# Kernel tuning notes

Measured on AMD Instinct MI355X. Metric: run time of the kernel, lower is better.

Reference implementation:

```python
import jax, jax.numpy as jnp
import numpy as np

D_MODEL = 768
NUM_HEADS = 12
D_K = D_MODEL // NUM_HEADS
B, S = 2, 4096


def setup_inputs() -> dict:
    key = jax.random.key(0)
    ks = jax.random.split(key, 11)
    lim = 1.0 / np.sqrt(D_MODEL)  # torch Linear default init range
    def lin(k1, k2):
        W = jax.random.uniform(k1, (D_MODEL, D_MODEL), jnp.float32, -lim, lim)
        b = jax.random.uniform(k2, (D_MODEL,), jnp.float32, -lim, lim)
        return W, b
    Wq, bq = lin(ks[0], ks[1])
    Wk, bk = lin(ks[2], ks[3])
    Wv, bv = lin(ks[4], ks[5])
    Wo, bo = lin(ks[6], ks[7])
    Q = jax.random.normal(ks[8], (B, S, D_MODEL), jnp.float32)
    K = jax.random.normal(ks[9], (B, S, D_MODEL), jnp.float32)
    V = jax.random.normal(ks[10], (B, S, D_MODEL), jnp.float32)
    return {"Q": Q, "K": K, "V": V,
            "Wq": Wq, "bq": bq, "Wk": Wk, "bk": bk,
            "Wv": Wv, "bv": bv, "Wo": Wo, "bo": bo}


def reference(Q, K, V, Wq, bq, Wk, bk, Wv, bv, Wo, bo):
    def split_heads(x):
        b, s, _ = x.shape
        return x.reshape(b, s, NUM_HEADS, D_K).transpose(0, 2, 1, 3)  # [B,H,S,d_k]

    q = split_heads(Q @ Wq.T + bq)
    k = split_heads(K @ Wk.T + bk)
    v = split_heads(V @ Wv.T + bv)

    scale = 1.0 / np.sqrt(D_K).astype(np.float32)
    scores = jnp.einsum('bhqd,bhkd->bhqk', q, k) * scale  # [B,H,S,S]
    probs = jax.nn.softmax(scores, axis=-1)
    attn = jnp.einsum('bhqk,bhkd->bhqd', probs, v)  # [B,H,S,d_k]

    out = attn.transpose(0, 2, 1, 3).reshape(Q.shape[0], Q.shape[1], D_MODEL)
    return out @ Wo.T + bo
```

## Files before the change

kernel.cpp:

```cpp
#include <hip/hip_runtime.h>
#include <hip/hip_bf16.h>
#include <stdint.h>

#define DM 768
#define DK 64
#define NH 12
#define SQ 4096
#define BB 2

typedef __attribute__((ext_vector_type(8))) short bf16x8;
typedef __attribute__((ext_vector_type(4))) float f32x4;
typedef __attribute__((ext_vector_type(16))) float f32x16;
typedef __attribute__((ext_vector_type(4))) unsigned short u16x4;
typedef __attribute__((ext_vector_type(4))) unsigned int u32x4;
typedef unsigned short u16;
typedef unsigned int   u32;

__device__ __forceinline__ u16 f2bf(float f) {
    u32 u = __builtin_bit_cast(u32, f);
    u32 r = (u + 0x7fffu + ((u >> 16) & 1u)) >> 16;
    return (u16)r;
}
__device__ __forceinline__ u32 pack_trunc(float lo, float hi) {
    return __builtin_amdgcn_perm(__builtin_bit_cast(u32, hi),
                                 __builtin_bit_cast(u32, lo), 0x07060302u);
}
__device__ __forceinline__ void gl_lds16(const u16* g, u16* l) {
    __builtin_amdgcn_global_load_lds(
        (const __attribute__((address_space(1))) void*)g,
        (__attribute__((address_space(3))) void*)l, 16, 0, 0);
}

__global__ __launch_bounds__(256) void cvt_w(
    const float* __restrict__ W0, const float* __restrict__ W1,
    const float* __restrict__ W2, const float* __restrict__ W3,
    u16* __restrict__ d0, u16* __restrict__ d1,
    u16* __restrict__ d2, u16* __restrict__ d3)
{
    const float* s = blockIdx.y == 0 ? W0 : blockIdx.y == 1 ? W1
                   : blockIdx.y == 2 ? W2 : W3;
    u16* d        = blockIdx.y == 0 ? d0 : blockIdx.y == 1 ? d1
                   : blockIdx.y == 2 ? d2 : d3;
    size_t i = ((size_t)blockIdx.x * 256 + threadIdx.x) * 8;
    float4 a = *(const float4*)&s[i];
    float4 b = *(const float4*)&s[i + 4];
    u16x4 lo, hi;
    lo.x = f2bf(a.x); lo.y = f2bf(a.y); lo.z = f2bf(a.z); lo.w = f2bf(a.w);
    hi.x = f2bf(b.x); hi.y = f2bf(b.y); hi.z = f2bf(b.z); hi.w = f2bf(b.w);
    *(u16x4*)&d[i]     = lo;
    *(u16x4*)&d[i + 4] = hi;
}

#define BM 128
#define BN 128

__global__ __launch_bounds__(256) void gemm_qkv(
    const float* __restrict__ A0, const float* __restrict__ A1,
    const float* __restrict__ A2,
    const u16* __restrict__ W0, const u16* __restrict__ W1,
    const u16* __restrict__ W2,
    const float* __restrict__ b0, const float* __restrict__ b1,
    const float* __restrict__ b2,
    u16* __restrict__ qo, u16* __restrict__ ko, u16* __restrict__ vto,
    float qscale)
{
    __shared__ __align__(16) u16 Asm[2][BM * 32];
    __shared__ __align__(16) u16 Bsm[2][BM * 32];

    const int tid  = threadIdx.x;
    const int lane = tid & 63;
    const int w    = tid >> 6;
    const int wr   = w >> 1, wc = w & 1;
    const int l16  = lane & 15, lg = lane >> 4;

    const int ntiles = DM / BN;
    const int mt = blockIdx.x / ntiles;
    const int nt = blockIdx.x % ntiles;
    const int m0 = mt * BM, n0 = nt * BN;

    const int op = blockIdx.y;
    const float* A    = op == 0 ? A0 : op == 1 ? A1 : A2;
    const u16*  W     = op == 0 ? W0 : op == 1 ? W1 : W2;
    const float* bias = op == 0 ? b0 : op == 1 ? b1 : b2;
    const float oscale = op == 0 ? qscale : 1.0f;

    f32x4 acc[4][4];
    #pragma unroll
    for (int mi = 0; mi < 4; ++mi)
        #pragma unroll
        for (int ni = 0; ni < 4; ++ni)
            #pragma unroll
            for (int r = 0; r < 4; ++r) acc[mi][ni][r] = 0.f;

    #define GSTAGE(K0, B)                                                      \
        do {                                                                   \
            _Pragma("unroll")                                                  \
            for (int i_ = 0; i_ < 2; ++i_) {                                   \
                int c_   = (i_ * 4 + w) * 64 + lane;                           \
                int row_ = c_ >> 2;                                            \
                int col_ = ((c_ & 3) ^ (row_ & 3)) * 8;                        \
                gl_lds16(&W[(size_t)(n0 + row_) * DM + (K0) + col_],           \
                         &Bsm[B][(i_ * 4 + w) * 512]);                         \
            }                                                                  \
            _Pragma("unroll")                                                  \
            for (int i_ = 0; i_ < 2; ++i_) {                                   \
                int s_   = tid + i_ * 256;                                     \
                int row_ = s_ >> 2;                                            \
                int col_ = ((s_ & 3) ^ (row_ & 3)) * 8;                        \
                float4 x_ = *(const float4*)&A[(size_t)(m0 + row_) * DM + (K0) + col_];     \
                float4 y_ = *(const float4*)&A[(size_t)(m0 + row_) * DM + (K0) + col_ + 4]; \
                u16x4 lo_, hi_;                                                \
                lo_.x = f2bf(x_.x); lo_.y = f2bf(x_.y);                        \
                lo_.z = f2bf(x_.z); lo_.w = f2bf(x_.w);                        \
                hi_.x = f2bf(y_.x); hi_.y = f2bf(y_.y);                        \
                hi_.z = f2bf(y_.z); hi_.w = f2bf(y_.w);                        \
                *(u16x4*)&Asm[B][s_ * 8]     = lo_;                            \
                *(u16x4*)&Asm[B][s_ * 8 + 4] = hi_;                            \
            }                                                                  \
        } while (0)

    GSTAGE(0, 0);

    for (int kk = 0; kk < DM / 32; ++kk) {
        __syncthreads();
        if (kk + 1 < DM / 32) GSTAGE((kk + 1) * 32, (kk + 1) & 1);

        const u16* Ab = Asm[kk & 1];
        const u16* Bb = Bsm[kk & 1];
        bf16x8 af[4], bfr[4];
        #pragma unroll
        for (int mi = 0; mi < 4; ++mi) {
            int r = wr * 64 + mi * 16 + l16;
            af[mi] = *(const bf16x8*)((const char*)Ab + (size_t)r * 64
                                      + (((lg ^ r) & 3) << 4));
        }
        #pragma unroll
        for (int ni = 0; ni < 4; ++ni) {
            int r = wc * 64 + ni * 16 + l16;
            bfr[ni] = *(const bf16x8*)((const char*)Bb + (size_t)r * 64
                                       + (((lg ^ r) & 3) << 4));
        }

        #pragma unroll
        for (int mi = 0; mi < 4; ++mi)
            #pragma unroll
            for (int ni = 0; ni < 4; ++ni)
                acc[mi][ni] = __builtin_amdgcn_mfma_f32_16x16x32_bf16(
                    af[mi], bfr[ni], acc[mi][ni], 0, 0, 0);
    }
    #undef GSTAGE

    #pragma unroll
    for (int mi = 0; mi < 4; ++mi)
        #pragma unroll
        for (int ni = 0; ni < 4; ++ni) {
            int n = n0 + wc * 64 + ni * 16 + l16;
            float bv = bias[n];
            if (op == 2) {
                int hh = n >> 6, dd = n & 63;
                int mb = m0 + wr * 64 + mi * 16 + lg * 4;
                int bI = mb >> 12;
                int kv = mb & (SQ - 1);
                u16x4 pk;
                #pragma unroll
                for (int r = 0; r < 4; ++r)
                    pk[r] = f2bf(acc[mi][ni][r] + bv);
                *(u16x4*)&vto[(((size_t)bI * NH + hh) * DK + dd) * SQ + kv] = pk;
            } else {
                u16* out = op ? ko : qo;
                #pragma unroll
                for (int r = 0; r < 4; ++r) {
                    int m = m0 + wr * 64 + mi * 16 + lg * 4 + r;
                    out[(size_t)m * DM + n] = f2bf((acc[mi][ni][r] + bv) * oscale);
                }
            }
        }
}

__global__ __launch_bounds__(256) void gemm_out(
    const u16* __restrict__ A, const u16* __restrict__ W,
    const float* __restrict__ bias, float* __restrict__ C)
{
    __shared__ __align__(16) u16 Asm[2][BM * 32];
    __shared__ __align__(16) u16 Bsm[2][BM * 32];

    const int tid  = threadIdx.x;
    const int lane = tid & 63;
    const int w    = tid >> 6;
    const int wr   = w >> 1, wc = w & 1;
    const int l16  = lane & 15, lg = lane >> 4;

    const int ntiles = DM / BN;
    const int mt = blockIdx.x / ntiles;
    const int nt = blockIdx.x % ntiles;
    const int m0 = mt * BM, n0 = nt * BN;

    f32x4 acc[4][4];
    #pragma unroll
    for (int mi = 0; mi < 4; ++mi)
        #pragma unroll
        for (int ni = 0; ni < 4; ++ni)
            #pragma unroll
            for (int r = 0; r < 4; ++r) acc[mi][ni][r] = 0.f;

    #define OSTAGE(K0, B)                                                      \
        do {                                                                   \
            _Pragma("unroll")                                                  \
            for (int i_ = 0; i_ < 2; ++i_) {                                   \
                int c_   = (i_ * 4 + w) * 64 + lane;                           \
                int row_ = c_ >> 2;                                            \
                int col_ = ((c_ & 3) ^ (row_ & 3)) * 8;                        \
                gl_lds16(&W[(size_t)(n0 + row_) * DM + (K0) + col_],           \
                         &Bsm[B][(i_ * 4 + w) * 512]);                         \
                gl_lds16(&A[(size_t)(m0 + row_) * DM + (K0) + col_],           \
                         &Asm[B][(i_ * 4 + w) * 512]);                         \
            }                                                                  \
        } while (0)

    OSTAGE(0, 0);

    for (int kk = 0; kk < DM / 32; ++kk) {
        __syncthreads();
        if (kk + 1 < DM / 32) OSTAGE((kk + 1) * 32, (kk + 1) & 1);

        const u16* Ab = Asm[kk & 1];
        const u16* Bb = Bsm[kk & 1];
        bf16x8 af[4], bfr[4];
        #pragma unroll
        for (int mi = 0; mi < 4; ++mi) {
            int r = wr * 64 + mi * 16 + l16;
            af[mi] = *(const bf16x8*)((const char*)Ab + (size_t)r * 64
                                      + (((lg ^ r) & 3) << 4));
        }
        #pragma unroll
        for (int ni = 0; ni < 4; ++ni) {
            int r = wc * 64 + ni * 16 + l16;
            bfr[ni] = *(const bf16x8*)((const char*)Bb + (size_t)r * 64
                                       + (((lg ^ r) & 3) << 4));
        }

        #pragma unroll
        for (int mi = 0; mi < 4; ++mi)
            #pragma unroll
            for (int ni = 0; ni < 4; ++ni)
                acc[mi][ni] = __builtin_amdgcn_mfma_f32_16x16x32_bf16(
                    af[mi], bfr[ni], acc[mi][ni], 0, 0, 0);
    }
    #undef OSTAGE

    #pragma unroll
    for (int mi = 0; mi < 4; ++mi)
        #pragma unroll
        for (int ni = 0; ni < 4; ++ni) {
            int n = n0 + wc * 64 + ni * 16 + l16;
            float bv = bias[n];
            #pragma unroll
            for (int r = 0; r < 4; ++r) {
                int m = m0 + wr * 64 + mi * 16 + lg * 4 + r;
                C[(size_t)m * DM + n] = acc[mi][ni][r] + bv;
            }
        }
}

__global__ __launch_bounds__(512) void flash_attn_db(
    const u16* __restrict__ Qm, const u16* __restrict__ Km,
    const u16* __restrict__ VT, u16* __restrict__ Om)
{
    __shared__ __align__(16) char ldsbuf[65536];

    const int tid  = threadIdx.x;
    const int lane = tid & 63;
    const int w    = tid >> 6;
    const int qg   = w & 3;
    const int half = w >> 2;
    const int kvL  = lane & 31;
    const int hi   = lane >> 5;

    const int qt = blockIdx.x;
    const int bh = blockIdx.y;
    const int b  = bh / NH, h = bh % NH;
    const size_t baseQ  = (size_t)b * SQ * DM + (size_t)h * DK;
    const size_t baseVT = (size_t)bh * DK * SQ;

    const int q = qt * 128 + qg * 32 + kvL;

    bf16x8 qf[4];
    #pragma unroll
    for (int j = 0; j < 4; ++j)
        qf[j] = *(const bf16x8*)&Qm[baseQ + (size_t)q * DM + j * 16 + hi * 8];

    int off[4];
    #pragma unroll
    for (int j = 0; j < 4; ++j)
        off[j] = kvL * 128 + (((2 * j + hi) ^ (kvL & 7)) << 4);

    int srow[2], schk[2];
    #pragma unroll
    for (int i = 0; i < 2; ++i) {
        int r = (qg * 2 + i) * 8 + (lane >> 3);
        srow[i] = r;
        schk[i] = (((lane & 7) ^ (r & 7)) << 3);
    }

    f32x16 accO[2];
    #pragma unroll
    for (int e = 0; e < 16; ++e) { accO[0][e] = 0.f; accO[1][e] = 0.f; }
    float lrun = 0.f;

    #define STAGE(T, B)                                                        \
        do {                                                                   \
            int kv0_ = (T) * 128 + half * 64;                                  \
            u16* KL_ = (u16*)(ldsbuf + (B) * 32768 + half * 16384);            \
            u16* VL_ = (u16*)(ldsbuf + (B) * 32768 + half * 16384 + 8192);     \
            _Pragma("unroll")                                                  \
            for (int i_ = 0; i_ < 2; ++i_) {                                   \
                gl_lds16(&Km[baseQ + (size_t)(kv0_ + srow[i_]) * DM + schk[i_]], \
                         KL_ + (qg * 2 + i_) * 512);                           \
                gl_lds16(&VT[baseVT + (size_t)srow[i_] * SQ + kv0_ + schk[i_]], \
                         VL_ + (qg * 2 + i_) * 512);                           \
            }                                                                  \
        } while (0)

    STAGE(0, 0);

    for (int t = 0; t < SQ / 128; ++t) {
        __syncthreads();
        if (t + 1 < SQ / 128) STAGE(t + 1, (t + 1) & 1);

        const char* KB = ldsbuf + (t & 1) * 32768 + half * 16384;
        const char* VB = KB + 8192;

        f32x16 s0, s1;
        #pragma unroll
        for (int e = 0; e < 16; ++e) { s0[e] = 0.f; s1[e] = 0.f; }
        __builtin_amdgcn_s_setprio(1);
        #pragma unroll
        for (int j = 0; j < 4; ++j) {
            bf16x8 kf0 = *(const bf16x8*)(KB + off[j]);
            bf16x8 kf1 = *(const bf16x8*)(KB + 4096 + off[j]);
            s0 = __builtin_amdgcn_mfma_f32_32x32x16_bf16(kf0, qf[j], s0, 0, 0, 0);
            s1 = __builtin_amdgcn_mfma_f32_32x32x16_bf16(kf1, qf[j], s1, 0, 0, 0);
        }
        __builtin_amdgcn_s_setprio(0);

        bf16x8 vf0[4], vf1[4];
        #pragma unroll
        for (int m = 0; m < 4; ++m) {
            vf0[m] = *(const bf16x8*)(VB + off[m]);
            vf1[m] = *(const bf16x8*)(VB + 4096 + off[m]);
        }

        u32 pb[16];
        float rs0 = 0.f, rs1 = 0.f;
        #pragma unroll
        for (int wd = 0; wd < 8; ++wd) {
            float a0 = __builtin_amdgcn_exp2f(s0[2 * wd]);
            float a1 = __builtin_amdgcn_exp2f(s0[2 * wd + 1]);
            float b0 = __builtin_amdgcn_exp2f(s1[2 * wd]);
            float b1 = __builtin_amdgcn_exp2f(s1[2 * wd + 1]);
            rs0 += a0 + a1;
            rs1 += b0 + b1;
            pb[wd]     = pack_trunc(a0, a1);
            pb[8 + wd] = pack_trunc(b0, b1);
        }
        lrun += rs0 + rs1;

        u32 snd[8], rcv[8];
        #pragma unroll
        for (int m = 0; m < 4; ++m) {
            int sb = 4 * m;
            snd[2 * m]     = hi ? pb[sb + 0] : pb[sb + 2];
            snd[2 * m + 1] = hi ? pb[sb + 1] : pb[sb + 3];
        }
        #pragma unroll
        for (int i = 0; i < 8; ++i)
            rcv[i] = (u32)__shfl_xor((int)snd[i], 32);

        __builtin_amdgcn_s_setprio(1);
        #pragma unroll
        for (int m = 0; m < 4; ++m) {
            int sb = 4 * m;
            u32x4 wds;
            wds[0] = hi ? rcv[2 * m]     : pb[sb + 0];
            wds[1] = hi ? rcv[2 * m + 1] : pb[sb + 1];
            wds[2] = hi ? pb[sb + 2]     : rcv[2 * m];
            wds[3] = hi ? pb[sb + 3]     : rcv[2 * m + 1];
            bf16x8 Bp = __builtin_bit_cast(bf16x8, wds);
            accO[0] = __builtin_amdgcn_mfma_f32_32x32x16_bf16(vf0[m], Bp, accO[0], 0, 0, 0);
            accO[1] = __builtin_amdgcn_mfma_f32_32x32x16_bf16(vf1[m], Bp, accO[1], 0, 0, 0);
        }
        __builtin_amdgcn_s_setprio(0);
    }
    #undef STAGE

    __syncthreads();

    lrun = lrun + __shfl_xor(lrun, 32);

    float* mo = (float*)ldsbuf;
    float* ml = (float*)(ldsbuf + 34816);
    const int rowi = (qg * 32 + kvL);

    if (half == 1) {
        float* row = mo + rowi * 68;
        #pragma unroll
        for (int c = 0; c < 2; ++c)
            #pragma unroll
            for (int e = 0; e < 16; ++e)
                row[(e >> 2) * 8 + (e & 3) + hi * 4 + c * 32] = accO[c][e];
        if (hi == 0) ml[rowi] = lrun;
    }
    __syncthreads();
    if (half == 0) {
        float* row = mo + rowi * 68;
        float inv = 1.f / (lrun + ml[rowi]);
        #pragma unroll
        for (int c = 0; c < 2; ++c)
            #pragma unroll
            for (int t4 = 0; t4 < 4; ++t4) {
                int d0 = t4 * 8 + hi * 4 + c * 32;
                u16x4 pk;
                #pragma unroll
                for (int u = 0; u < 4; ++u) {
                    float val = (accO[c][t4 * 4 + u] + row[d0 + u]) * inv;
                    pk[u] = f2bf(val);
                }
                *(u16x4*)&Om[baseQ + (size_t)q * DM + d0] = pk;
            }
    }
}

extern "C" void kernel_launch(void* const* d_in, const int* in_sizes, int n_in,
                              void* d_out, int out_size, void* d_ws, size_t ws_size,
                              hipStream_t stream)
{
    const float* Q  = (const float*)d_in[0];
    const float* K  = (const float*)d_in[1];
    const float* V  = (const float*)d_in[2];
    const float* Wq = (const float*)d_in[3];
    const float* bq = (const float*)d_in[4];
    const float* Wk = (const float*)d_in[5];
    const float* bk = (const float*)d_in[6];
    const float* Wv = (const float*)d_in[7];
    const float* bv = (const float*)d_in[8];
    const float* Wo = (const float*)d_in[9];
    const float* bo = (const float*)d_in[10];
    (void)in_sizes; (void)n_in; (void)out_size; (void)ws_size;

    const size_t E  = (size_t)BB * SQ * DM;
    const size_t WE = (size_t)DM * DM;
    u16* qws  = (u16*)d_ws;
    u16* kws  = qws + E;
    u16* vtws = kws + E;
    u16* aws  = vtws + E;
    u16* wqb  = aws + E;
    u16* wkb  = wqb + WE;
    u16* wvb  = wkb + WE;
    u16* wob  = wvb + WE;

    const float qscale = 0.125f * 1.4426950408889634f;

    hipLaunchKernelGGL(cvt_w, dim3(WE / 2048, 4), dim3(256), 0, stream,
                       Wq, Wk, Wv, Wo, wqb, wkb, wvb, wob);

    dim3 gq((BB * SQ / BM) * (DM / BN), 3);
    hipLaunchKernelGGL(gemm_qkv, gq, dim3(256), 0, stream,
                       Q, K, V, wqb, wkb, wvb, bq, bk, bv,
                       qws, kws, vtws, qscale);

    dim3 ga(SQ / 128, BB * NH);
    hipLaunchKernelGGL(flash_attn_db, ga, dim3(512), 0, stream, qws, kws, vtws, aws);

    dim3 gg((BB * SQ / BM) * (DM / BN));
    hipLaunchKernelGGL(gemm_out, gg, dim3(256), 0, stream, aws, wob, bo, (float*)d_out);
}
```

Measured before the change: 241.7 us.

## Permute V transpose layout to drop cross-lane shuffles in PV MFMA

The V projection epilogue now writes the transposed V with a swizzled kv index (bits 2 and 3 swapped). The attention kernel's P fragments then already match the MFMA B-operand layout, so the eight shfl_xor exchanges between lane halves per tile are removed. V fragment loads also move next to their MFMAs, which lowers register pressure but may expose LDS latency.

```diff
diff --git a/kernel.cpp b/kernel.cpp
--- a/kernel.cpp
+++ b/kernel.cpp
@@ -161,11 +161,12 @@
                 int mb = m0 + wr * 64 + mi * 16 + lg * 4;
                 int bI = mb >> 12;
                 int kv = mb & (SQ - 1);
+                int kvs = (kv & ~12) | ((kv & 4) << 1) | ((kv & 8) >> 1);
                 u16x4 pk;
                 #pragma unroll
                 for (int r = 0; r < 4; ++r)
                     pk[r] = f2bf(acc[mi][ni][r] + bv);
-                *(u16x4*)&vto[(((size_t)bI * NH + hh) * DK + dd) * SQ + kv] = pk;
+                *(u16x4*)&vto[(((size_t)bI * NH + hh) * DK + dd) * SQ + kvs] = pk;
             } else {
                 u16* out = op ? ko : qo;
                 #pragma unroll
@@ -343,13 +344,6 @@
         }
         __builtin_amdgcn_s_setprio(0);
 
-        bf16x8 vf0[4], vf1[4];
-        #pragma unroll
-        for (int m = 0; m < 4; ++m) {
-            vf0[m] = *(const bf16x8*)(VB + off[m]);
-            vf1[m] = *(const bf16x8*)(VB + 4096 + off[m]);
-        }
-
         u32 pb[16];
         float rs0 = 0.f, rs1 = 0.f;
         #pragma unroll
@@ -365,29 +359,20 @@
         }
         lrun += rs0 + rs1;
 
-        u32 snd[8], rcv[8];
-        #pragma unroll
-        for (int m = 0; m < 4; ++m) {
-            int sb = 4 * m;
-            snd[2 * m]     = hi ? pb[sb + 0] : pb[sb + 2];
-            snd[2 * m + 1] = hi ? pb[sb + 1] : pb[sb + 3];
-        }
-        #pragma unroll
-        for (int i = 0; i < 8; ++i)
-            rcv[i] = (u32)__shfl_xor((int)snd[i], 32);
-
         __builtin_amdgcn_s_setprio(1);
         #pragma unroll
         for (int m = 0; m < 4; ++m) {
             int sb = 4 * m;
             u32x4 wds;
-            wds[0] = hi ? rcv[2 * m]     : pb[sb + 0];
-            wds[1] = hi ? rcv[2 * m + 1] : pb[sb + 1];
-            wds[2] = hi ? pb[sb + 2]     : rcv[2 * m];
-            wds[3] = hi ? pb[sb + 3]     : rcv[2 * m + 1];
+            wds[0] = pb[sb + 0];
+            wds[1] = pb[sb + 1];
+            wds[2] = pb[sb + 2];
+            wds[3] = pb[sb + 3];
             bf16x8 Bp = __builtin_bit_cast(bf16x8, wds);
-            accO[0] = __builtin_amdgcn_mfma_f32_32x32x16_bf16(vf0[m], Bp, accO[0], 0, 0, 0);
-            accO[1] = __builtin_amdgcn_mfma_f32_32x32x16_bf16(vf1[m], Bp, accO[1], 0, 0, 0);
+            bf16x8 v0 = *(const bf16x8*)(VB + off[m]);
+            bf16x8 v1 = *(const bf16x8*)(VB + 4096 + off[m]);
+            accO[0] = __builtin_amdgcn_mfma_f32_32x32x16_bf16(v0, Bp, accO[0], 0, 0, 0);
+            accO[1] = __builtin_amdgcn_mfma_f32_32x32x16_bf16(v1, Bp, accO[1], 0, 0, 0);
         }
         __builtin_amdgcn_s_setprio(0);
     }
```

Result: faster. 225.0 us (-6.9%).
